# Optimization experiments

Measured on AMD Instinct MI355X. Metric: run time of the kernel, lower is better.

Reference implementation:

```python
import jax, jax.numpy as jnp
import numpy as np

N = 50000          # nodes
E = 1_600_000      # directed edges (avg degree 32)
C_IN = 512
C_OUT = 64
H1, F1 = 8, 8      # conv1: heads=8, out per head=8
H2 = 1             # conv2: heads_2=1, concat=False
NEG_SLOPE = 0.2    # GATConv default leaky_relu slope
ELU_ALPHA = 0.2    # F.elu(..., alpha=0.2) in forward


def _glorot(key, shape):
    fan_in, fan_out = shape[0], shape[-1]
    lim = jnp.sqrt(6.0 / (fan_in + fan_out))
    return jax.random.uniform(key, shape, jnp.float32, -lim, lim)


def setup_inputs() -> dict:
    key = jax.random.key(0)
    ks = jax.random.split(key, 12)
    x = jax.random.normal(ks[0], (N, C_IN), jnp.float32)
    edge_index = jax.random.randint(ks[1], (2, E), 0, N, jnp.int32)
    # conv1 params
    W1 = _glorot(ks[2], (C_IN, H1 * F1))
    att_src1 = _glorot(ks[3], (H1, F1))
    att_dst1 = _glorot(ks[4], (H1, F1))
    b1 = jnp.zeros((H1 * F1,), jnp.float32)
    # conv2 params (concat=False, heads=1)
    W2 = _glorot(ks[5], (H1 * F1, H2 * C_OUT))
    att_src2 = _glorot(ks[6], (H2, C_OUT))
    att_dst2 = _glorot(ks[7], (H2, C_OUT))
    b2 = jnp.zeros((C_OUT,), jnp.float32)
    return dict(x=x, edge_index=edge_index, W1=W1, att_src1=att_src1,
                att_dst1=att_dst1, b1=b1, W2=W2, att_src2=att_src2,
                att_dst2=att_dst2, b2=b2)


def gat_conv(x, src, dst, W, att_src, att_dst, bias, concat):
    """PyG GATConv (self-loops already appended to src/dst). Eval mode (no dropout)."""
    n = x.shape[0]
    H, F = att_src.shape
    h = (x @ W).reshape(n, H, F)                       # [N,H,F]
    a_src = jnp.sum(h * att_src, axis=-1)              # [N,H]
    a_dst = jnp.sum(h * att_dst, axis=-1)              # [N,H]
    e = jax.nn.leaky_relu(a_src[src] + a_dst[dst], NEG_SLOPE)  # [E',H]
    # segment softmax over incoming edges of each destination node
    m = jax.ops.segment_max(e, dst, num_segments=n)    # [N,H]
    m = jnp.where(jnp.isfinite(m), m, 0.0)
    ex = jnp.exp(e - m[dst])
    denom = jax.ops.segment_sum(ex, dst, num_segments=n)
    alpha = ex / (denom[dst] + 1e-16)                  # [E',H]
    msg = h[src] * alpha[:, :, None]                   # [E',H,F]
    out = jax.ops.segment_sum(msg, dst, num_segments=n)  # [N,H,F]
    out = out.reshape(n, H * F) if concat else out.mean(axis=1)
    return out + bias


def reference(x, edge_index, W1, att_src1, att_dst1, b1,
              W2, att_src2, att_dst2, b2):
    # add self loops once (GATConv default add_self_loops=True)
    loop = jnp.arange(N, dtype=edge_index.dtype)
    src = jnp.concatenate([edge_index[0], loop])
    dst = jnp.concatenate([edge_index[1], loop])
    # dropout layers are identity in eval mode
    h = gat_conv(x, src, dst, W1, att_src1, att_dst1, b1, concat=True)
    h = jax.nn.elu(h, alpha=ELU_ALPHA)
    out = gat_conv(h, src, dst, W2, att_src2, att_dst2, b2, concat=False)
    return out
```

## Files before the change

kernel.cpp:

```cpp
#include <hip/hip_runtime.h>
#include <hip/hip_bf16.h>
#include <hip/hip_fp16.h>

constexpr int NN   = 50000;
constexpr int NE   = 1600000;
constexpr int CIN  = 512;
constexpr int DH   = 64;
constexpr int H1N  = 8;

constexpr int NB     = 98;
constexpr int TILE   = 8192;
constexpr int NTILES = (NE + TILE - 1) / TILE;
constexpr int BCAP   = 20480;

typedef __attribute__((ext_vector_type(8))) short bf16x8v;
typedef __attribute__((ext_vector_type(4))) float f32x4v;

__device__ __forceinline__ float bf(unsigned short u) {
    union { unsigned int i; float f; } v; v.i = ((unsigned int)u) << 16; return v.f;
}
__device__ __forceinline__ float lrelu(float x) { return fmaxf(x, 0.2f * x); }
__device__ __forceinline__ float ldf(const unsigned short* p, size_t i, bool f32) {
    return f32 ? ((const float*)p)[i] : bf(p[i]);
}
__device__ __forceinline__ unsigned short f2bf(float f) {
    union { float f; unsigned int u; } v; v.f = f;
    unsigned int r = (v.u + 0x7fff + ((v.u >> 16) & 1)) >> 16;
    return (unsigned short)r;
}

__global__ __launch_bounds__(256) void gat_detect(const unsigned short* __restrict__ W1,
                                                  int* __restrict__ flag) {
    __shared__ int cnt;
    if (threadIdx.x == 0) cnt = 0;
    __syncthreads();
    int local = 0;
    for (int i = threadIdx.x; i < 4096; i += 256) {
        unsigned short u = W1[i];
        int e = (u >> 7) & 0xFF;
        if (e >= 140) local++;
    }
    atomicAdd(&cnt, local);
    __syncthreads();
    if (threadIdx.x == 0) flag[0] = (cnt > 100) ? 1 : 0;
}


__global__ __launch_bounds__(256) void gat_bucketA(const int* __restrict__ src,
                                                   const int* __restrict__ dst,
                                                   int* __restrict__ gcnt,
                                                   unsigned int* __restrict__ bucketed) {
    __shared__ int hist[NB];
    __shared__ int cur[NB];
    int t = threadIdx.x;
    if (t < NB) hist[t] = 0;
    __syncthreads();
    int base = blockIdx.x * TILE;
    for (int i = t; i < TILE; i += 256) {
        int e = base + i;
        if (e < NE) atomicAdd(&hist[dst[e] >> 9], 1);
    }
    __syncthreads();
    if (t < NB) cur[t] = hist[t] ? atomicAdd(&gcnt[t], hist[t]) : 0;
    __syncthreads();
    for (int i = t; i < TILE; i += 256) {
        int e = base + i;
        if (e < NE) {
            int d = dst[e];
            int b = d >> 9;
            int p = atomicAdd(&cur[b], 1);
            if (p < BCAP)
                bucketed[(size_t)b * BCAP + p] =
                    ((unsigned int)(d & 511) << 16) | (unsigned int)src[e];
        }
    }
}

__global__ __launch_bounds__(128) void gat_bucketscan(const int* __restrict__ gcnt,
                                                      int* __restrict__ boff,
                                                      int* __restrict__ row_ptr) {
    __shared__ int s[128];
    int t = threadIdx.x;
    s[t] = (t < NB) ? gcnt[t] : 0;
    __syncthreads();
    for (int off = 1; off < 128; off <<= 1) {
        int x = s[t];
        int add = (t >= off) ? s[t - off] : 0;
        __syncthreads();
        s[t] = x + add;
        __syncthreads();
    }
    if (t <= NB) boff[t] = (t == 0) ? 0 : s[t - 1];
    if (t == 0) row_ptr[NN] = NE;
}

__global__ __launch_bounds__(256) void gat_bucketB(const unsigned int* __restrict__ bucketed,
                                                   const int* __restrict__ gcnt,
                                                   const int* __restrict__ boff,
                                                   int* __restrict__ row_ptr,
                                                   int* __restrict__ col_idx) {
    __shared__ int hist[512];
    __shared__ int sums[256];
    int t = threadIdx.x;
    int b = blockIdx.x;
    int e0 = boff[b];
    int cnt = gcnt[b]; if (cnt > BCAP) cnt = BCAP;
    const unsigned int* bb = bucketed + (size_t)b * BCAP;
    hist[t] = 0; hist[t + 256] = 0;
    __syncthreads();
    for (int i = t; i < cnt; i += 256)
        atomicAdd(&hist[bb[i] >> 16], 1);
    __syncthreads();
    int a0 = hist[2 * t], a1 = hist[2 * t + 1];
    sums[t] = a0 + a1;
    __syncthreads();
    for (int off = 1; off < 256; off <<= 1) {
        int x = sums[t];
        int add = (t >= off) ? sums[t - off] : 0;
        __syncthreads();
        sums[t] = x + add;
        __syncthreads();
    }
    int excl = (t == 0) ? 0 : sums[t - 1];
    hist[2 * t]     = excl;
    hist[2 * t + 1] = excl + a0;
    int node0 = b << 9;
    if (node0 + 2 * t     < NN) row_ptr[node0 + 2 * t]     = e0 + excl;
    if (node0 + 2 * t + 1 < NN) row_ptr[node0 + 2 * t + 1] = e0 + excl + a0;
    __syncthreads();
    for (int i = t; i < cnt; i += 256) {
        unsigned int pk = bb[i];
        int p = atomicAdd(&hist[pk >> 16], 1);
        col_idx[e0 + p] = (int)(pk & 0xFFFFu);
    }
}


__global__ __launch_bounds__(256) void gat_maxcol(const float* __restrict__ v, int n, int H,
                                                  unsigned int* __restrict__ out) {
    __shared__ float red[256];
    int t = threadIdx.x;
    float mx = -3.4e38f;
    for (int idx = blockIdx.x * 256 + t; idx < n; idx += gridDim.x * 256)
        mx = fmaxf(mx, v[idx]);
    red[t] = mx;
    __syncthreads();
    for (int off = 128; off >= H; off >>= 1) {
        if (t < off) red[t] = fmaxf(red[t], red[t + off]);
        __syncthreads();
    }
    if (t < H) {
        union { float f; unsigned int u; } b; b.f = red[t];
        unsigned int enc = (b.u & 0x80000000u) ? ~b.u : (b.u | 0x80000000u);
        atomicMax(&out[t], enc);
    }
}

__device__ __forceinline__ float gdecode(unsigned int u) {
    union { unsigned int u; float f; } d;
    d.u = (u & 0x80000000u) ? (u ^ 0x80000000u) : ~u;
    return d.f;
}


__global__ __launch_bounds__(256) void gat_transW(const unsigned short* __restrict__ W1,
                                                  const int* __restrict__ flag,
                                                  unsigned short* __restrict__ wts) {
    int idx = blockIdx.x * 256 + threadIdx.x;
    int n = idx >> 9, k = idx & 511;
    if (flag[0] == 0) {
        int o  = n * 1024 + k * 2;
        int os = o ^ ((n & 7) << 4);
        wts[os >> 1] = W1[(size_t)k * DH + n];
    } else {
        float v = ((const float*)W1)[(size_t)k * DH + n];
        unsigned short hi = f2bf(v);
        union { unsigned int u; float f; } hf; hf.u = ((unsigned int)hi) << 16;
        unsigned short lo = f2bf(v - hf.f);
        int half = k >> 8, kk = k & 255;
        int o = half * 65536 + n * 512 + ((kk * 2) ^ ((n & 7) << 4));
        wts[o >> 1]             = hi;
        wts[(o + 32768) >> 1]   = lo;
    }
}


__global__ __launch_bounds__(256) void gat_gemm1_mfma(const unsigned short* __restrict__ x,
                                                      const unsigned short* __restrict__ wts,
                                                      const unsigned short* __restrict__ as1,
                                                      const unsigned short* __restrict__ ad1,
                                                      const int* __restrict__ flag,
                                                      __half* __restrict__ h1h,
                                                      float* __restrict__ a_s1,
                                                      float* __restrict__ a_d1) {
    if (flag[0] != 0) return;
    __shared__ __align__(16) unsigned short wl[32768];
    int t = threadIdx.x;
#pragma unroll
    for (int it = 0; it < 16; ++it) {
        int c = it * 256 + t;
        *(uint4*)((char*)wl + c * 16) = *(const uint4*)((const char*)wts + c * 16);
    }
    __syncthreads();

    int lane = t & 63, wv = t >> 6;
    int g = lane >> 4;
    int r = lane & 15;
    int chunk = blockIdx.x * 4 + wv;
    if (chunk * 16 >= NN) return;
    int rowbase = chunk * 16;

    int vbase = r * 1024;
    int gx = g * 16;
    int xr = (r & 7) << 4;

    const char* xrow = (const char*)x + ((size_t)(rowbase + r) * CIN + g * 8) * 2;

    f32x4v acc[4];
#pragma unroll
    for (int nt = 0; nt < 4; ++nt) acc[nt] = (f32x4v){0.f, 0.f, 0.f, 0.f};

#pragma unroll 4
    for (int s = 0; s < 16; ++s) {
        union { uint4 u; bf16x8v v; } a;
        a.u = *(const uint4*)(xrow + s * 64);
        int o = vbase + ((s * 64 + gx) ^ xr);
        const char* bp = (const char*)wl + o;
#pragma unroll
        for (int nt = 0; nt < 4; ++nt) {
            union { uint4 u; bf16x8v v; } bv;
            bv.u = *(const uint4*)(bp + nt * 16384);
            acc[nt] = __builtin_amdgcn_mfma_f32_16x16x32_bf16(a.v, bv.v, acc[nt], 0, 0, 0);
        }
    }

    float avs[4], avd[4];
#pragma unroll
    for (int nt = 0; nt < 4; ++nt) {
        avs[nt] = bf(as1[nt * 16 + r]);
        avd[nt] = bf(ad1[nt * 16 + r]);
    }

#pragma unroll
    for (int nt = 0; nt < 4; ++nt) {
#pragma unroll
        for (int i = 0; i < 4; ++i) {
            int row = rowbase + g * 4 + i;
            float v = acc[nt][i];
            h1h[(size_t)row * DH + nt * 16 + r] = __float2half(v);
            float ps = v * avs[nt];
            float pd = v * avd[nt];
            ps += __shfl_xor(ps, 1, 64); ps += __shfl_xor(ps, 2, 64); ps += __shfl_xor(ps, 4, 64);
            pd += __shfl_xor(pd, 1, 64); pd += __shfl_xor(pd, 2, 64); pd += __shfl_xor(pd, 4, 64);
            if ((r & 7) == 0) {
                int head = nt * 2 + (r >> 3);
                a_s1[row * H1N + head] = ps;
                a_d1[row * H1N + head] = pd;
            }
        }
    }
}


__global__ __launch_bounds__(256) void gat_gemm1_mfma_f32(const float* __restrict__ x,
                                                          const unsigned short* __restrict__ wts,
                                                          const float* __restrict__ as1,
                                                          const float* __restrict__ ad1,
                                                          const int* __restrict__ flag,
                                                          __half* __restrict__ h1h,
                                                          float* __restrict__ a_s1,
                                                          float* __restrict__ a_d1) {
    if (flag[0] == 0) return;
    __shared__ __align__(16) unsigned short wl[32768];
    int t = threadIdx.x;
    int lane = t & 63, wv = t >> 6;
    int g = lane >> 4;
    int r = lane & 15;
    int chunk = blockIdx.x * 4 + wv;
    bool active = (chunk * 16 < NN);
    int rowbase = (active ? chunk : 0) * 16;

    int vbase = r * 512;
    int xr = (r & 7) << 4;

    const float* xrow = x + (size_t)(rowbase + r) * CIN + g * 8;

    f32x4v acc[4];
#pragma unroll
    for (int nt = 0; nt < 4; ++nt) acc[nt] = (f32x4v){0.f, 0.f, 0.f, 0.f};

    for (int half = 0; half < 2; ++half) {
        if (half) __syncthreads();
        const uint4* gsrc = (const uint4*)((const char*)wts + half * 65536);
#pragma unroll
        for (int it = 0; it < 16; ++it)
            ((uint4*)wl)[it * 256 + t] = gsrc[it * 256 + t];
        __syncthreads();

#pragma unroll 2
        for (int s = 0; s < 8; ++s) {
            const float4* xp = (const float4*)(xrow + half * 256 + s * 32);
            float4 v0 = xp[0], v1 = xp[1];
            float xv[8] = {v0.x, v0.y, v0.z, v0.w, v1.x, v1.y, v1.z, v1.w};
            union { unsigned short u[8]; bf16x8v v; } ahi, alo;
#pragma unroll
            for (int i2 = 0; i2 < 8; ++i2) {
                union { float f; unsigned int u; } xb; xb.f = xv[i2];
                unsigned int hb = xb.u & 0xffff0000u;
                union { unsigned int u; float f; } hf; hf.u = hb;
                ahi.u[i2] = (unsigned short)(xb.u >> 16);
                alo.u[i2] = f2bf(xv[i2] - hf.f);
            }
            int o = vbase + ((s * 64 + g * 16) ^ xr);
#pragma unroll
            for (int nt = 0; nt < 4; ++nt) {
                union { uint4 u; bf16x8v v; } bhi, blo;
                bhi.u = *(const uint4*)((const char*)wl + nt * 8192 + o);
                blo.u = *(const uint4*)((const char*)wl + 32768 + nt * 8192 + o);
                acc[nt] = __builtin_amdgcn_mfma_f32_16x16x32_bf16(ahi.v, bhi.v, acc[nt], 0, 0, 0);
                acc[nt] = __builtin_amdgcn_mfma_f32_16x16x32_bf16(ahi.v, blo.v, acc[nt], 0, 0, 0);
                acc[nt] = __builtin_amdgcn_mfma_f32_16x16x32_bf16(alo.v, bhi.v, acc[nt], 0, 0, 0);
            }
        }
    }

    if (!active) return;

    float avs[4], avd[4];
#pragma unroll
    for (int nt = 0; nt < 4; ++nt) {
        avs[nt] = as1[nt * 16 + r];
        avd[nt] = ad1[nt * 16 + r];
    }

#pragma unroll
    for (int nt = 0; nt < 4; ++nt) {
#pragma unroll
        for (int i = 0; i < 4; ++i) {
            int row = rowbase + g * 4 + i;
            float v = acc[nt][i];
            h1h[(size_t)row * DH + nt * 16 + r] = __float2half(v);
            float ps = v * avs[nt];
            float pd = v * avd[nt];
            ps += __shfl_xor(ps, 1, 64); ps += __shfl_xor(ps, 2, 64); ps += __shfl_xor(ps, 4, 64);
            pd += __shfl_xor(pd, 1, 64); pd += __shfl_xor(pd, 2, 64); pd += __shfl_xor(pd, 4, 64);
            if ((r & 7) == 0) {
                int head = nt * 2 + (r >> 3);
                a_s1[row * H1N + head] = ps;
                a_d1[row * H1N + head] = pd;
            }
        }
    }
}


__global__ __launch_bounds__(256) void gat_agg1(const int* __restrict__ row_ptr,
                                                const int* __restrict__ col_idx,
                                                const float* __restrict__ a_s1,
                                                const float* __restrict__ a_d1,
                                                const unsigned int* __restrict__ Gsu,
                                                const __half* __restrict__ h1h,
                                                const unsigned short* __restrict__ b1,
                                                const int* __restrict__ flag,
                                                float* __restrict__ hout) {
    const bool f32 = (flag[0] != 0);
    int i = (blockIdx.x * 256 + threadIdx.x) >> 6;
    int lane = threadIdx.x & 63;
    if (i >= NN) return;
    int ek = lane & 3;
    int eh = (lane >> 2) & 7;
    int wbase = (lane >> 3) << 2;

    float adst = a_d1[i * H1N + eh];
    float m = lrelu(gdecode(Gsu[eh]) + adst);

    int jb = row_ptr[i], je = row_ptr[i + 1];
    int deg = je - jb;
    int myidx = (lane < deg) ? col_idx[jb + lane] : 0;

    float wself = __expf(lrelu(a_s1[i * H1N + eh] + adst) - m);
    float denp = (ek == 0) ? wself : 0.f;
    float wsb = __shfl(wself, wbase, 64);
    float acc = wsb * __half2float(h1h[(size_t)i * DH + lane]);

    for (int j0 = 0; j0 < deg; j0 += 4) {
        int s0, s1, s2, s3, se;
        bool vE = (j0 + ek) < deg;
        if (j0 < 64) {
            s0 = __shfl(myidx, j0,     64);
            s1 = __shfl(myidx, j0 + 1, 64);
            s2 = __shfl(myidx, j0 + 2, 64);
            s3 = __shfl(myidx, j0 + 3, 64);
            se = __shfl(myidx, j0 + ek, 64);
        } else {
            int j1 = j0 + 1 < deg ? j0 + 1 : j0;
            int j2 = j0 + 2 < deg ? j0 + 2 : j0;
            int j3 = j0 + 3 < deg ? j0 + 3 : j0;
            int jve = vE ? (j0 + ek) : j0;
            s0 = col_idx[jb + j0];
            s1 = col_idx[jb + j1];
            s2 = col_idx[jb + j2];
            s3 = col_idx[jb + j3];
            se = col_idx[jb + jve];
        }
        float w = __expf(lrelu(a_s1[se * H1N + eh] + adst) - m);
        w = vE ? w : 0.f;
        denp += w;
        float w0 = __shfl(w, wbase + 0, 64);
        float w1 = __shfl(w, wbase + 1, 64);
        float w2 = __shfl(w, wbase + 2, 64);
        float w3 = __shfl(w, wbase + 3, 64);
        float r0 = __half2float(h1h[(size_t)s0 * DH + lane]);
        float r1 = __half2float(h1h[(size_t)s1 * DH + lane]);
        float r2 = __half2float(h1h[(size_t)s2 * DH + lane]);
        float r3 = __half2float(h1h[(size_t)s3 * DH + lane]);
        acc += (w0 * r0 + w1 * r1) + (w2 * r2 + w3 * r3);
    }
    denp += __shfl_xor(denp, 1, 64);
    denp += __shfl_xor(denp, 2, 64);
    float denom = __shfl(denp, wbase, 64);

    float val = acc / denom + ldf(b1, lane, f32);
    val = val > 0.f ? val : 0.2f * (__expf(val) - 1.f);
    hout[(size_t)i * DH + lane] = val;
}


__global__ __launch_bounds__(256) void gat_gemm2(const float* __restrict__ hin,
                                                 const unsigned short* __restrict__ W2,
                                                 const unsigned short* __restrict__ as2,
                                                 const unsigned short* __restrict__ ad2,
                                                 const int* __restrict__ flag,
                                                 __half* __restrict__ h2h,
                                                 float* __restrict__ a_s2,
                                                 float* __restrict__ a_d2) {
    __shared__ float w2[DH * DH];
    const bool f32 = (flag[0] != 0);
    int t = threadIdx.x;
    int lane = t & 63, wv = t >> 6;
    for (int idx = t; idx < DH * DH; idx += 256) w2[idx] = ldf(W2, idx, f32);
    __syncthreads();

    float asv = ldf(as2, lane, f32);
    float adv = ldf(ad2, lane, f32);

    int stride = gridDim.x * 4;
    for (int row = blockIdx.x * 4 + wv; row < NN; row += stride) {
        const float* hr = hin + (size_t)row * DH;
        float acc = 0.f;
#pragma unroll 8
        for (int k = 0; k < DH; ++k) acc += hr[k] * w2[k * DH + lane];
        h2h[(size_t)row * DH + lane] = __float2half(acc);
        float ps = acc * asv, pd = acc * adv;
#pragma unroll
        for (int o = 1; o < 64; o <<= 1) {
            ps += __shfl_xor(ps, o, 64);
            pd += __shfl_xor(pd, o, 64);
        }
        if (lane == 0) { a_s2[row] = ps; a_d2[row] = pd; }
    }
}


__global__ __launch_bounds__(256) void gat_agg2(const int* __restrict__ row_ptr,
                                                const int* __restrict__ col_idx,
                                                const float* __restrict__ a_s2,
                                                const float* __restrict__ a_d2,
                                                const unsigned int* __restrict__ Gsu2,
                                                const __half* __restrict__ h2h,
                                                const unsigned short* __restrict__ b2,
                                                const int* __restrict__ flag,
                                                void* __restrict__ out) {
    const bool f32 = (flag[0] != 0);
    int i = (blockIdx.x * 256 + threadIdx.x) >> 6;
    int lane = threadIdx.x & 63;
    if (i >= NN) return;
    int ek = lane & 3;

    float adst = a_d2[i];
    float m = lrelu(gdecode(Gsu2[0]) + adst);

    int jb = row_ptr[i], je = row_ptr[i + 1];
    int deg = je - jb;
    int myidx = (lane < deg) ? col_idx[jb + lane] : 0;

    float wself = __expf(lrelu(a_s2[i] + adst) - m);
    float denp = (ek == 0) ? wself : 0.f;
    float acc = wself * __half2float(h2h[(size_t)i * DH + lane]);

    for (int j0 = 0; j0 < deg; j0 += 4) {
        int s0, s1, s2, s3, se;
        bool vE = (j0 + ek) < deg;
        if (j0 < 64) {
            s0 = __shfl(myidx, j0,     64);
            s1 = __shfl(myidx, j0 + 1, 64);
            s2 = __shfl(myidx, j0 + 2, 64);
            s3 = __shfl(myidx, j0 + 3, 64);
            se = __shfl(myidx, j0 + ek, 64);
        } else {
            int j1 = j0 + 1 < deg ? j0 + 1 : j0;
            int j2 = j0 + 2 < deg ? j0 + 2 : j0;
            int j3 = j0 + 3 < deg ? j0 + 3 : j0;
            int jve = vE ? (j0 + ek) : j0;
            s0 = col_idx[jb + j0];
            s1 = col_idx[jb + j1];
            s2 = col_idx[jb + j2];
            s3 = col_idx[jb + j3];
            se = col_idx[jb + jve];
        }
        float w = __expf(lrelu(a_s2[se] + adst) - m);
        w = vE ? w : 0.f;
        denp += w;
        float w0 = __shfl(w, 0, 64);
        float w1 = __shfl(w, 1, 64);
        float w2 = __shfl(w, 2, 64);
        float w3 = __shfl(w, 3, 64);
        float r0 = __half2float(h2h[(size_t)s0 * DH + lane]);
        float r1 = __half2float(h2h[(size_t)s1 * DH + lane]);
        float r2 = __half2float(h2h[(size_t)s2 * DH + lane]);
        float r3 = __half2float(h2h[(size_t)s3 * DH + lane]);
        acc += (w0 * r0 + w1 * r1) + (w2 * r2 + w3 * r3);
    }
    denp += __shfl_xor(denp, 1, 64);
    denp += __shfl_xor(denp, 2, 64);
    float denom = __shfl(denp, 0, 64);

    float val = acc / denom + ldf(b2, lane, f32);
    size_t oi = (size_t)i * DH + lane;
    if (f32) ((float*)out)[oi] = val;
    else     ((__hip_bfloat16*)out)[oi] = __float2bfloat16(val);
}


static void* g_scratch = nullptr;

extern "C" void kernel_launch(void* const* d_in, const int* in_sizes, int n_in,
                              void* d_out, int out_size, void* d_ws, size_t ws_size,
                              hipStream_t stream) {
    const unsigned short* x   = (const unsigned short*)d_in[0];
    const int*            ei  = (const int*)d_in[1];
    const unsigned short* W1  = (const unsigned short*)d_in[2];
    const unsigned short* as1 = (const unsigned short*)d_in[3];
    const unsigned short* ad1 = (const unsigned short*)d_in[4];
    const unsigned short* b1  = (const unsigned short*)d_in[5];
    const unsigned short* W2  = (const unsigned short*)d_in[6];
    const unsigned short* as2 = (const unsigned short*)d_in[7];
    const unsigned short* ad2 = (const unsigned short*)d_in[8];
    const unsigned short* b2  = (const unsigned short*)d_in[9];

    const int* srcv = ei;
    const int* dstv = ei + NE;

    const size_t off_wts   = 64;
    const size_t off_h1h   = off_wts + 131072;
    const size_t off_hmid  = off_h1h + (size_t)NN * DH * 2;
    const size_t off_as1   = off_hmid + (size_t)NN * DH * 4;
    const size_t off_ad1   = off_as1 + (size_t)NN * H1N * 4;
    const size_t off_rp    = off_ad1 + (size_t)NN * H1N * 4;
    const size_t off_ci    = off_rp + (size_t)(NN + 1) * 4;
    const size_t off_bk    = off_ci + (size_t)NE * 4;
    const size_t off_gcnt  = off_bk + (size_t)NB * BCAP * 4;
    const size_t off_gsu   = off_gcnt + 128 * 4;
    const size_t off_boff  = off_gsu + 16 * 4;
    const size_t need      = off_boff + 128 * 4;

    void* wsbase = d_ws;
    if (ws_size < need) {
        if (g_scratch == nullptr) hipMalloc(&g_scratch, need);
        wsbase = g_scratch;
    }
    char* B = (char*)wsbase;

    int*            flag = (int*)B;
    unsigned short* wts  = (unsigned short*)(B + off_wts);
    __half*         h1h  = (__half*)(B + off_h1h);
    float*          hmid = (float*)(B + off_hmid);
    float*          a_s1 = (float*)(B + off_as1);
    float*          a_d1 = (float*)(B + off_ad1);
    int*         row_ptr = (int*)(B + off_rp);
    int*         col_idx = (int*)(B + off_ci);
    unsigned int* bucketed = (unsigned int*)(B + off_bk);
    int*            gcnt = (int*)(B + off_gcnt);
    unsigned int*   Gsu  = (unsigned int*)(B + off_gsu);
    int*            boff = (int*)(B + off_boff);
    __half* h2h  = h1h;
    float* a_s2 = a_s1;
    float* a_d2 = a_d1;

    hipMemsetAsync(gcnt, 0, (128 + 16) * sizeof(int), stream);
    gat_detect<<<1, 256, 0, stream>>>(W1, flag);

    gat_bucketA   <<<NTILES, 256, 0, stream>>>(srcv, dstv, gcnt, bucketed);
    gat_bucketscan<<<1, 128, 0, stream>>>(gcnt, boff, row_ptr);
    gat_bucketB   <<<NB, 256, 0, stream>>>(bucketed, gcnt, boff, row_ptr, col_idx);

    gat_transW<<<128, 256, 0, stream>>>(W1, flag, wts);
    int gemmb = (3125 + 3) / 4;
    gat_gemm1_mfma    <<<gemmb, 256, 0, stream>>>(x, wts, as1, ad1, flag, h1h, a_s1, a_d1);
    gat_gemm1_mfma_f32<<<gemmb, 256, 0, stream>>>((const float*)x, wts,
                                                  (const float*)as1, (const float*)ad1,
                                                  flag, h1h, a_s1, a_d1);

    gat_maxcol<<<64, 256, 0, stream>>>(a_s1, NN * H1N, 8, Gsu);

    int nb = (NN * 64 + 255) / 256;
    gat_agg1<<<nb, 256, 0, stream>>>(row_ptr, col_idx, a_s1, a_d1, Gsu, h1h, b1, flag, hmid);

    gat_gemm2<<<512, 256, 0, stream>>>(hmid, W2, as2, ad2, flag, h2h, a_s2, a_d2);

    gat_maxcol<<<32, 256, 0, stream>>>(a_s2, NN, 1, Gsu + 8);

    gat_agg2<<<nb, 256, 0, stream>>>(row_ptr, col_idx, a_s2, a_d2, Gsu + 8, h2h, b2, flag, d_out);
}
```

Baseline: 459.8 us.

## Move second GEMM to split-bf16 MFMA and shrink gemm1 fp32 LDS staging

```diff
diff --git a/kernel.cpp b/kernel.cpp
--- a/kernel.cpp
+++ b/kernel.cpp
@@ -177,11 +177,33 @@
         unsigned short hi = f2bf(v);
         union { unsigned int u; float f; } hf; hf.u = ((unsigned int)hi) << 16;
         unsigned short lo = f2bf(v - hf.f);
-        int half = k >> 8, kk = k & 255;
-        int o = half * 65536 + n * 512 + ((kk * 2) ^ ((n & 7) << 4));
+        int q = k >> 7, kk = k & 127;
+        int o = q * 32768 + n * 256 + ((kk * 2) ^ ((n & 7) << 4));
         wts[o >> 1]             = hi;
-        wts[(o + 32768) >> 1]   = lo;
-    }
+        wts[(o + 16384) >> 1]   = lo;
+    }
+}
+
+
+__global__ __launch_bounds__(256) void gat_transW2(const unsigned short* __restrict__ W2,
+                                                   const int* __restrict__ flag,
+                                                   unsigned short* __restrict__ wts2) {
+    int idx = blockIdx.x * 256 + threadIdx.x;
+    if (idx >= 4096) return;
+    int n = idx & 63, k = idx >> 6;
+    unsigned short hi, lo;
+    if (flag[0] == 0) {
+        hi = W2[(size_t)k * DH + n];
+        lo = 0;
+    } else {
+        float v = ((const float*)W2)[(size_t)k * DH + n];
+        hi = f2bf(v);
+        union { unsigned int u; float f; } hf; hf.u = ((unsigned int)hi) << 16;
+        lo = f2bf(v - hf.f);
+    }
+    int o = n * 128 + ((k * 2) ^ ((n & 7) << 4));
+    wts2[o >> 1]            = hi;
+    wts2[(o + 8192) >> 1]   = lo;
 }
 
 
@@ -271,7 +293,7 @@
                                                           float* __restrict__ a_s1,
                                                           float* __restrict__ a_d1) {
     if (flag[0] == 0) return;
-    __shared__ __align__(16) unsigned short wl[32768];
+    __shared__ __align__(16) unsigned short wl[16384];
     int t = threadIdx.x;
     int lane = t & 63, wv = t >> 6;
     int g = lane >> 4;
@@ -280,7 +302,7 @@
     bool active = (chunk * 16 < NN);
     int rowbase = (active ? chunk : 0) * 16;
 
-    int vbase = r * 512;
+    int vbase = r * 256;
     int xr = (r & 7) << 4;
 
     const float* xrow = x + (size_t)(rowbase + r) * CIN + g * 8;
@@ -289,17 +311,17 @@
 #pragma unroll
     for (int nt = 0; nt < 4; ++nt) acc[nt] = (f32x4v){0.f, 0.f, 0.f, 0.f};
 
-    for (int half = 0; half < 2; ++half) {
-        if (half) __syncthreads();
-        const uint4* gsrc = (const uint4*)((const char*)wts + half * 65536);
-#pragma unroll
-        for (int it = 0; it < 16; ++it)
+    for (int q = 0; q < 4; ++q) {
+        if (q) __syncthreads();
+        const uint4* gsrc = (const uint4*)((const char*)wts + q * 32768);
+#pragma unroll
+        for (int it = 0; it < 8; ++it)
             ((uint4*)wl)[it * 256 + t] = gsrc[it * 256 + t];
         __syncthreads();
 
-#pragma unroll 2
-        for (int s = 0; s < 8; ++s) {
-            const float4* xp = (const float4*)(xrow + half * 256 + s * 32);
+#pragma unroll
+        for (int s = 0; s < 4; ++s) {
+            const float4* xp = (const float4*)(xrow + q * 128 + s * 32);
             float4 v0 = xp[0], v1 = xp[1];
             float xv[8] = {v0.x, v0.y, v0.z, v0.w, v1.x, v1.y, v1.z, v1.w};
             union { unsigned short u[8]; bf16x8v v; } ahi, alo;
@@ -315,8 +337,8 @@
 #pragma unroll
             for (int nt = 0; nt < 4; ++nt) {
                 union { uint4 u; bf16x8v v; } bhi, blo;
-                bhi.u = *(const uint4*)((const char*)wl + nt * 8192 + o);
-                blo.u = *(const uint4*)((const char*)wl + 32768 + nt * 8192 + o);
+                bhi.u = *(const uint4*)((const char*)wl + nt * 4096 + o);
+                blo.u = *(const uint4*)((const char*)wl + 16384 + nt * 4096 + o);
                 acc[nt] = __builtin_amdgcn_mfma_f32_16x16x32_bf16(ahi.v, bhi.v, acc[nt], 0, 0, 0);
                 acc[nt] = __builtin_amdgcn_mfma_f32_16x16x32_bf16(ahi.v, blo.v, acc[nt], 0, 0, 0);
                 acc[nt] = __builtin_amdgcn_mfma_f32_16x16x32_bf16(alo.v, bhi.v, acc[nt], 0, 0, 0);
@@ -426,38 +448,87 @@
 }
 
 
-__global__ __launch_bounds__(256) void gat_gemm2(const float* __restrict__ hin,
-                                                 const unsigned short* __restrict__ W2,
-                                                 const unsigned short* __restrict__ as2,
-                                                 const unsigned short* __restrict__ ad2,
-                                                 const int* __restrict__ flag,
-                                                 __half* __restrict__ h2h,
-                                                 float* __restrict__ a_s2,
-                                                 float* __restrict__ a_d2) {
-    __shared__ float w2[DH * DH];
+__global__ __launch_bounds__(256) void gat_gemm2_mfma(const float* __restrict__ hin,
+                                                      const unsigned short* __restrict__ wts2,
+                                                      const unsigned short* __restrict__ as2,
+                                                      const unsigned short* __restrict__ ad2,
+                                                      const int* __restrict__ flag,
+                                                      __half* __restrict__ h2h,
+                                                      float* __restrict__ a_s2,
+                                                      float* __restrict__ a_d2) {
+    __shared__ __align__(16) unsigned short wl[8192];
     const bool f32 = (flag[0] != 0);
     int t = threadIdx.x;
+#pragma unroll
+    for (int it = 0; it < 4; ++it)
+        ((uint4*)wl)[it * 256 + t] = ((const uint4*)wts2)[it * 256 + t];
+    __syncthreads();
+
     int lane = t & 63, wv = t >> 6;
-    for (int idx = t; idx < DH * DH; idx += 256) w2[idx] = ldf(W2, idx, f32);
-    __syncthreads();
-
-    float asv = ldf(as2, lane, f32);
-    float adv = ldf(ad2, lane, f32);
-
-    int stride = gridDim.x * 4;
-    for (int row = blockIdx.x * 4 + wv; row < NN; row += stride) {
-        const float* hr = hin + (size_t)row * DH;
-        float acc = 0.f;
-#pragma unroll 8
-        for (int k = 0; k < DH; ++k) acc += hr[k] * w2[k * DH + lane];
-        h2h[(size_t)row * DH + lane] = __float2half(acc);
-        float ps = acc * asv, pd = acc * adv;
-#pragma unroll
-        for (int o = 1; o < 64; o <<= 1) {
-            ps += __shfl_xor(ps, o, 64);
-            pd += __shfl_xor(pd, o, 64);
-        }
-        if (lane == 0) { a_s2[row] = ps; a_d2[row] = pd; }
+    int g = lane >> 4;
+    int r = lane & 15;
+    int chunk = blockIdx.x * 4 + wv;
+    if (chunk * 16 >= NN) return;
+    int rowbase = chunk * 16;
+
+    int vbase = r * 128;
+    int xr = (r & 7) << 4;
+
+    const float* xrow = hin + (size_t)(rowbase + r) * DH + g * 8;
+
+    f32x4v acc[4];
+#pragma unroll
+    for (int nt = 0; nt < 4; ++nt) acc[nt] = (f32x4v){0.f, 0.f, 0.f, 0.f};
+
+#pragma unroll
+    for (int s = 0; s < 2; ++s) {
+        const float4* xp = (const float4*)(xrow + s * 32);
+        float4 v0 = xp[0], v1 = xp[1];
+        float xv[8] = {v0.x, v0.y, v0.z, v0.w, v1.x, v1.y, v1.z, v1.w};
+        union { unsigned short u[8]; bf16x8v v; } ahi, alo;
+#pragma unroll
+        for (int i2 = 0; i2 < 8; ++i2) {
+            union { float f; unsigned int u; } xb; xb.f = xv[i2];
+            unsigned int hb = xb.u & 0xffff0000u;
+            union { unsigned int u; float f; } hf; hf.u = hb;
+            ahi.u[i2] = (unsigned short)(xb.u >> 16);
+            alo.u[i2] = f2bf(xv[i2] - hf.f);
+        }
+        int o = vbase + ((s * 64 + g * 16) ^ xr);
+#pragma unroll
+        for (int nt = 0; nt < 4; ++nt) {
+            union { uint4 u; bf16x8v v; } bhi, blo;
+            bhi.u = *(const uint4*)((const char*)wl + nt * 2048 + o);
+            blo.u = *(const uint4*)((const char*)wl + 8192 + nt * 2048 + o);
+            acc[nt] = __builtin_amdgcn_mfma_f32_16x16x32_bf16(ahi.v, bhi.v, acc[nt], 0, 0, 0);
+            acc[nt] = __builtin_amdgcn_mfma_f32_16x16x32_bf16(ahi.v, blo.v, acc[nt], 0, 0, 0);
+            acc[nt] = __builtin_amdgcn_mfma_f32_16x16x32_bf16(alo.v, bhi.v, acc[nt], 0, 0, 0);
+        }
+    }
+
+    float avs[4], avd[4];
+#pragma unroll
+    for (int nt = 0; nt < 4; ++nt) {
+        avs[nt] = ldf(as2, nt * 16 + r, f32);
+        avd[nt] = ldf(ad2, nt * 16 + r, f32);
+    }
+
+#pragma unroll
+    for (int i = 0; i < 4; ++i) {
+        int row = rowbase + g * 4 + i;
+        float ps = 0.f, pd = 0.f;
+#pragma unroll
+        for (int nt = 0; nt < 4; ++nt) {
+            float v = acc[nt][i];
+            h2h[(size_t)row * DH + nt * 16 + r] = __float2half(v);
+            ps += v * avs[nt];
+            pd += v * avd[nt];
+        }
+        ps += __shfl_xor(ps, 1, 64); ps += __shfl_xor(ps, 2, 64);
+        ps += __shfl_xor(ps, 4, 64); ps += __shfl_xor(ps, 8, 64);
+        pd += __shfl_xor(pd, 1, 64); pd += __shfl_xor(pd, 2, 64);
+        pd += __shfl_xor(pd, 4, 64); pd += __shfl_xor(pd, 8, 64);
+        if (r == 0) { a_s2[row] = ps; a_d2[row] = pd; }
     }
 }
 
@@ -552,7 +623,8 @@
     const int* dstv = ei + NE;
 
     const size_t off_wts   = 64;
-    const size_t off_h1h   = off_wts + 131072;
+    const size_t off_wts2  = off_wts + 131072;
+    const size_t off_h1h   = off_wts2 + 16384;
     const size_t off_hmid  = off_h1h + (size_t)NN * DH * 2;
     const size_t off_as1   = off_hmid + (size_t)NN * DH * 4;
     const size_t off_ad1   = off_as1 + (size_t)NN * H1N * 4;
@@ -573,6 +645,7 @@
 
     int*            flag = (int*)B;
     unsigned short* wts  = (unsigned short*)(B + off_wts);
+    unsigned short* wts2 = (unsigned short*)(B + off_wts2);
     __half*         h1h  = (__half*)(B + off_h1h);
     float*          hmid = (float*)(B + off_hmid);
     float*          a_s1 = (float*)(B + off_as1);
@@ -594,7 +667,8 @@
     gat_bucketscan<<<1, 128, 0, stream>>>(gcnt, boff, row_ptr);
     gat_bucketB   <<<NB, 256, 0, stream>>>(bucketed, gcnt, boff, row_ptr, col_idx);
 
-    gat_transW<<<128, 256, 0, stream>>>(W1, flag, wts);
+    gat_transW <<<128, 256, 0, stream>>>(W1, flag, wts);
+    gat_transW2<<<16, 256, 0, stream>>>(W2, flag, wts2);
     int gemmb = (3125 + 3) / 4;
     gat_gemm1_mfma    <<<gemmb, 256, 0, stream>>>(x, wts, as1, ad1, flag, h1h, a_s1, a_d1);
     gat_gemm1_mfma_f32<<<gemmb, 256, 0, stream>>>((const float*)x, wts,
@@ -606,7 +680,7 @@
     int nb = (NN * 64 + 255) / 256;
     gat_agg1<<<nb, 256, 0, stream>>>(row_ptr, col_idx, a_s1, a_d1, Gsu, h1h, b1, flag, hmid);
 
-    gat_gemm2<<<512, 256, 0, stream>>>(hmid, W2, as2, ad2, flag, h2h, a_s2, a_d2);
+    gat_gemm2_mfma<<<gemmb, 256, 0, stream>>>(hmid, wts2, as2, ad2, flag, h2h, a_s2, a_d2);
 
     gat_maxcol<<<32, 256, 0, stream>>>(a_s2, NN, 1, Gsu + 8);
 
```

New measurement: 420.6 us. 1.09x faster.
